# Performance work log

Measured on AMD Instinct MI355X. Metric: run time of the kernel, lower is better.

Reference implementation:

```python
import jax, jax.numpy as jnp
import numpy as np

B, Q, K = 16, 100, 100
H, DM = 8, 512
DK = DM // H          # 64, per-head dim (= Attention embed_dim)
MID = 32              # mid_dim
EPS = 1e-5            # GroupNorm eps
NEG = -1000000000.0   # masked_fill value


def setup_inputs() -> dict:
    key = jax.random.key(0)
    ks = jax.random.split(key, 32)
    def n(k, shape, s=0.02):
        return jax.random.normal(k, shape, jnp.float32) * s
    inp = {
        "query": jax.random.normal(ks[0], (B, Q, DM), jnp.float32),
        "key":   jax.random.normal(ks[1], (B, K, DM), jnp.float32),
        "value": jax.random.normal(ks[2], (B, K, DM), jnp.float32),
        "mask":  jnp.ones((B, Q, K), jnp.float32),
        # 4 input projections: Linear(DM,DM) -> CELU -> GroupNorm(H, DM)
        "Wq1": n(ks[3], (DM, DM)), "bq1": jnp.zeros((DM,), jnp.float32),
        "gw1": jnp.ones((DM,), jnp.float32), "gb1": jnp.zeros((DM,), jnp.float32),
        "Wk":  n(ks[4], (DM, DM)), "bk":  jnp.zeros((DM,), jnp.float32),
        "gwk": jnp.ones((DM,), jnp.float32), "gbk": jnp.zeros((DM,), jnp.float32),
        "Wq2": n(ks[5], (DM, DM)), "bq2": jnp.zeros((DM,), jnp.float32),
        "gw2": jnp.ones((DM,), jnp.float32), "gb2": jnp.zeros((DM,), jnp.float32),
        "Wv":  n(ks[6], (DM, DM)), "bv":  jnp.zeros((DM,), jnp.float32),
        "gwv": jnp.ones((DM,), jnp.float32), "gbv": jnp.zeros((DM,), jnp.float32),
        # Attention MLPs (per-head, embed_dim = DK)
        "We":  n(ks[7], (MID, DK)), "be":  jnp.zeros((MID,), jnp.float32),
        "Ws":  n(ks[8], (1, MID)),  "bs":  jnp.zeros((1,), jnp.float32),
        "Wsq": n(ks[9], (DK, MID)), "bsq": jnp.zeros((DK,), jnp.float32),
    }
    return inp


def _proj(x, W, b, gw, gb):
    """Linear -> CELU -> GroupNorm(H groups over DM channels), then split heads.
    x: (B, L, DM) -> (B, H, L, DK)"""
    Bn, L, _ = x.shape
    y = jax.nn.celu(x.reshape(Bn * L, DM) @ W.T + b)
    yg = y.reshape(Bn * L, H, DK)
    mu = yg.mean(-1, keepdims=True)
    var = yg.var(-1, keepdims=True)
    yn = ((yg - mu) * jax.lax.rsqrt(var + EPS)).reshape(Bn * L, DM)
    yn = yn * gw + gb
    return yn.reshape(Bn, L, H, DK).transpose(0, 2, 1, 3)


def reference(query, key, value, mask,
              Wq1, bq1, gw1, gb1, Wk, bk, gwk, gbk,
              Wq2, bq2, gw2, gb2, Wv, bv, gwv, gbv,
              We, be, Ws, bs, Wsq, bsq):
    q1 = _proj(query, Wq1, bq1, gw1, gb1)   # (B,H,Q,DK)
    k  = _proj(key,   Wk,  bk,  gwk, gbk)   # (B,H,K,DK)
    q2 = _proj(query, Wq2, bq2, gw2, gb2)   # (B,H,Q,DK)
    v  = _proj(value, Wv,  bv,  gwv, gbv)   # (B,H,K,DK)

    m = mask[:, None]                        # (B,1,Q,K)
    # bilinear query-key map, embedded by Linear->ReLU (dropout=identity, eval)
    key_map = jnp.einsum('bhqd,bhkd->bhqkd', q1, k)          # (B,H,Q,K,DK)
    km = jax.nn.relu(jnp.einsum('bhqkd,md->bhqkm', key_map, We) + be)  # (B,H,Q,K,MID)

    alpha = jnp.einsum('bhqkm,m->bhqk', km, Ws[0]) + bs[0]   # (B,H,Q,K)
    alpha = jnp.where(m == 0, NEG, alpha)
    alpha = jax.nn.softmax(alpha, axis=-1)

    # masked mean pooling over K, then channel squeeze-excite
    pool = jnp.sum(km * m[..., None], axis=-2) / jnp.sum(m[..., None], axis=-2)  # (B,H,Q,MID)
    ch = jax.nn.sigmoid(pool @ Wsq.T + bsq)                  # (B,H,Q,DK)

    # spatial attention over val_map: sum_k alpha * (q2_d * v_kd) = q2 * (alpha @ v)
    sp = q2 * jnp.einsum('bhqk,bhkd->bhqd', alpha, v)        # (B,H,Q,DK)
    x = sp * ch
    return x.transpose(0, 2, 1, 3).reshape(x.shape[0], -1, DM)  # (B,Q,DM)
```

## Files before the change

### kernel.cpp

```cpp
#include <hip/hip_runtime.h>
#include <hip/hip_bf16.h>
#include <math.h>

#define H 8
#define DM 512
#define DK 64
#define MID 32
#define LL 100
#define EPS 1e-5f
#define NEGV -1000000000.0f

typedef unsigned short u16;
typedef __attribute__((ext_vector_type(8))) short short8b;
typedef __attribute__((ext_vector_type(16))) float f32x16;

#define MFMA32 __builtin_amdgcn_mfma_f32_32x32x16_bf16

__device__ __forceinline__ unsigned pkbf2(float a, float b) {
    union { __hip_bfloat162 h; unsigned u; } cv;
    cv.h = __float22bfloat162_rn(make_float2(a, b));
    return cv.u;
}
__device__ __forceinline__ u16 bfbits(float a) {
    union { __hip_bfloat16 b; u16 u; } cv;
    cv.b = __float2bfloat16(a);
    return cv.u;
}
__device__ __forceinline__ float bf2f(u16 u) {
    union { u16 u; __hip_bfloat16 b; } cv; cv.u = u;
    return __bfloat162float(cv.b);
}

__global__ __launch_bounds__(256) void cvt_kernel(
    const float* __restrict__ q, const float* __restrict__ k, const float* __restrict__ v,
    const float* __restrict__ w1, const float* __restrict__ wk,
    const float* __restrict__ w2, const float* __restrict__ wv,
    u16* __restrict__ qh, u16* __restrict__ qlo, u16* __restrict__ kh, u16* __restrict__ klo,
    u16* __restrict__ vh, u16* __restrict__ vlo,
    u16* __restrict__ w1h, u16* __restrict__ w1l, u16* __restrict__ wkh, u16* __restrict__ wkl,
    u16* __restrict__ w2h, u16* __restrict__ w2l, u16* __restrict__ wvh, u16* __restrict__ wvl)
{
    int g = blockIdx.x * 256 + threadIdx.x;
    const float* src; u16 *dh, *dl; int off;
    if (g < 307200) {
        int a = g / 102400;
        off = g - a * 102400;
        src = a == 0 ? q : (a == 1 ? k : v);
        dh  = a == 0 ? qh : (a == 1 ? kh : vh);
        dl  = a == 0 ? qlo : (a == 1 ? klo : vlo);
    } else {
        int gg = g - 307200;
        int a = gg >> 15;
        off = gg & 32767;
        src = a == 0 ? w1 : (a == 1 ? wk : (a == 2 ? w2 : wv));
        dh  = a == 0 ? w1h : (a == 1 ? wkh : (a == 2 ? w2h : wvh));
        dl  = a == 0 ? w1l : (a == 1 ? wkl : (a == 2 ? w2l : wvl));
    }
    const int rr = off & 31, hf = (off >> 5) & 1, kb = (off >> 6) & 31, tile = off >> 11;
    const float* sp = src + ((size_t)(tile * 32 + rr)) * 512 + kb * 16 + hf * 8;
    float4 x0 = *(const float4*)sp;
    float4 x1 = *(const float4*)(sp + 4);
    float xs[8] = {x0.x, x0.y, x0.z, x0.w, x1.x, x1.y, x1.z, x1.w};
    u16 hb[8], lb[8];
    #pragma unroll
    for (int j = 0; j < 8; ++j) {
        hb[j] = bfbits(xs[j]);
        lb[j] = bfbits(xs[j] - bf2f(hb[j]));
    }
    ushort4 h0; h0.x = hb[0]; h0.y = hb[1]; h0.z = hb[2]; h0.w = hb[3];
    ushort4 h1; h1.x = hb[4]; h1.y = hb[5]; h1.z = hb[6]; h1.w = hb[7];
    ushort4 l0; l0.x = lb[0]; l0.y = lb[1]; l0.z = lb[2]; l0.w = lb[3];
    ushort4 l1; l1.x = lb[4]; l1.y = lb[5]; l1.z = lb[6]; l1.w = lb[7];
    *(ushort4*)(dh + (size_t)off * 8)     = h0;
    *(ushort4*)(dh + (size_t)off * 8 + 4) = h1;
    *(ushort4*)(dl + (size_t)off * 8)     = l0;
    *(ushort4*)(dl + (size_t)off * 8 + 4) = l1;
}

__global__ __launch_bounds__(256) void proj_kernel(
    const u16* __restrict__ qh, const u16* __restrict__ qlo,
    const u16* __restrict__ kh, const u16* __restrict__ klo,
    const u16* __restrict__ vh, const u16* __restrict__ vlo,
    const u16* __restrict__ w1h, const u16* __restrict__ w1l,
    const u16* __restrict__ wkh, const u16* __restrict__ wkl,
    const u16* __restrict__ w2h, const u16* __restrict__ w2l,
    const u16* __restrict__ wvh, const u16* __restrict__ wvl,
    const float* __restrict__ bq1, const float* __restrict__ gw1, const float* __restrict__ gb1,
    const float* __restrict__ bk , const float* __restrict__ gwk, const float* __restrict__ gbk,
    const float* __restrict__ bq2, const float* __restrict__ gw2, const float* __restrict__ gb2,
    const float* __restrict__ bv , const float* __restrict__ gwv, const float* __restrict__ gbv,
    float* __restrict__ q1o, u16* __restrict__ kbf,
    float* __restrict__ q2o, u16* __restrict__ vtbf)
{
    __shared__ float lds_s[4][32];
    __shared__ float lds_q[4][32];

    const int rt = blockIdx.x;
    const int ct = blockIdx.y;
    const int p  = blockIdx.z;
    const int t = threadIdx.x, w = t >> 6, lane = t & 63, ql = lane & 31, hf = lane >> 5;
    const int wr = w >> 1, wc = w & 1;

    const u16 *Xhg, *Xlg, *Whg, *Wlg; const float *bias, *gw, *gb;
    if (p == 0)      { Xhg=qh; Xlg=qlo; Whg=w1h; Wlg=w1l; bias=bq1; gw=gw1; gb=gb1; }
    else if (p == 1) { Xhg=kh; Xlg=klo; Whg=wkh; Wlg=wkl; bias=bk;  gw=gwk; gb=gbk; }
    else if (p == 2) { Xhg=qh; Xlg=qlo; Whg=w2h; Wlg=w2l; bias=bq2; gw=gw2; gb=gb2; }
    else             { Xhg=vh; Xlg=vlo; Whg=wvh; Wlg=wvl; bias=bv;  gw=gwv; gb=gbv; }

    const int rtile = rt * 2 + wr;
    const int ctile = ct * 2 + wc;
    const u16* pAh = Xhg + (size_t)rtile * 16384 + hf * 256 + ql * 8;
    const u16* pAl = Xlg + (size_t)rtile * 16384 + hf * 256 + ql * 8;
    const u16* pBh = Whg + (size_t)ctile * 16384 + hf * 256 + ql * 8;
    const u16* pBl = Wlg + (size_t)ctile * 16384 + hf * 256 + ql * 8;

    f32x16 acc = {0.f,0.f,0.f,0.f,0.f,0.f,0.f,0.f,0.f,0.f,0.f,0.f,0.f,0.f,0.f,0.f};
    #pragma unroll 4
    for (int kb = 0; kb < 32; ++kb) {
        short8b Ah = *(const short8b*)(pAh + kb * 512);
        short8b Al = *(const short8b*)(pAl + kb * 512);
        short8b Bh = *(const short8b*)(pBh + kb * 512);
        short8b Bl = *(const short8b*)(pBl + kb * 512);
        acc = MFMA32(Ah, Bh, acc, 0, 0, 0);
        acc = MFMA32(Ah, Bl, acc, 0, 0, 0);
        acc = MFMA32(Al, Bh, acc, 0, 0, 0);
    }

    const int colg = ct * 64 + wc * 32 + ql;
    const float bv_ = bias[colg];
    const float gwc = gw[colg], gbc = gb[colg];
    float y[16], s[16], sq[16];
    #pragma unroll
    for (int r = 0; r < 16; ++r) {
        float x = acc[r] + bv_;
        x = x > 0.f ? x : expm1f(x);
        y[r] = x; s[r] = x; sq[r] = x * x;
    }
    #pragma unroll
    for (int off = 1; off < 32; off <<= 1) {
        #pragma unroll
        for (int r = 0; r < 16; ++r) {
            s[r]  += __shfl_xor(s[r],  off, 64);
            sq[r] += __shfl_xor(sq[r], off, 64);
        }
    }
    if (ql == 0) {
        #pragma unroll
        for (int r = 0; r < 16; ++r) {
            int row = (r & 3) + 8 * (r >> 2) + 4 * hf;
            lds_s[w][row] = s[r]; lds_q[w][row] = sq[r];
        }
    }
    __syncthreads();
    const int wp = w ^ 1;
    const int hh = ct, dk = wc * 32 + ql;
    const int r0 = rt * 64 + wr * 32;
    #pragma unroll
    for (int r = 0; r < 16; ++r) {
        int row = (r & 3) + 8 * (r >> 2) + 4 * hf;
        float sum = lds_s[w][row] + lds_s[wp][row];
        float ssq = lds_q[w][row] + lds_q[wp][row];
        float mu  = sum * (1.f / 64.f);
        float var = ssq * (1.f / 64.f) - mu * mu;
        float inv = rsqrtf(var + EPS);
        float yn  = (y[r] - mu) * inv * gwc + gbc;
        int rg = r0 + row;
        int b = rg / 100;
        int l = rg - b * 100;
        size_t bh = (size_t)(b * H + hh);
        if (p == 0)      q1o[(bh * 100 + l) * 64 + dk] = yn;
        else if (p == 2) q2o[(bh * 100 + l) * 64 + dk] = yn;
        else if (p == 1) kbf[(bh * 128 + l) * 64 + dk] = bfbits(yn);
        else             vtbf[(bh * 64 + dk) * 128 + l] = bfbits(yn);
    }
}

__global__ __launch_bounds__(256, 2) void attn_kernel(
    const float* __restrict__ q1o, const u16* __restrict__ kbf,
    const float* __restrict__ q2o, const u16* __restrict__ vtbf,
    const float* __restrict__ mask,
    const float* __restrict__ We, const float* __restrict__ be,
    const float* __restrict__ Wsv, const float* __restrict__ bs,
    const float* __restrict__ Wsq, const float* __restrict__ bsq,
    float* __restrict__ out)
{
    __shared__ float lds_We[32 * 64];
    __shared__ float lds_score[128 * 33];
    __shared__ float lds_pool[2][32 * 33];
    __shared__ float lds_of[2][16 * 64];
    __shared__ float lds_mx[2][32], lds_se[2][32], lds_ms[2][32];

    const int bh = blockIdx.x, b = bh >> 3, h = bh & 7, qt = blockIdx.y;
    const int tid = threadIdx.x;
    const int w = tid >> 6, lane = tid & 63;
    const int wk = w >> 1, wm = w & 1;
    const int ql = lane & 31, hf = lane >> 5;
    const int q0 = qt * 32, q = q0 + ql;
    const int qc = q < 100 ? q : 99;

    for (int i = tid * 4; i < 2048; i += 1024)
        *(float4*)(lds_We + i) = *(const float4*)(We + i);
    for (int i = tid; i < 2 * 32 * 33; i += 256)
        ((float*)lds_pool)[i] = 0.f;

    const u16* kb = kbf + (size_t)bh * 128 * 64;
    short8b A[2][4];
    #pragma unroll
    for (int mtl = 0; mtl < 2; ++mtl)
        #pragma unroll
        for (int ks = 0; ks < 4; ++ks)
            A[mtl][ks] = *(const short8b*)(kb + (size_t)((2 * wk + mtl) * 32 + ql) * 64 + ks * 16 + hf * 8);

    float q1r[4][8];
    const float* q1p = q1o + ((size_t)bh * 100 + qc) * 64;
    #pragma unroll
    for (int ks = 0; ks < 4; ++ks) {
        float4 u0 = *(const float4*)(q1p + ks * 16 + hf * 8);
        float4 u1 = *(const float4*)(q1p + ks * 16 + hf * 8 + 4);
        q1r[ks][0] = u0.x; q1r[ks][1] = u0.y; q1r[ks][2] = u0.z; q1r[ks][3] = u0.w;
        q1r[ks][4] = u1.x; q1r[ks][5] = u1.y; q1r[ks][6] = u1.z; q1r[ks][7] = u1.w;
    }
    const float bsv = bs[0];

    float sc[2][16];
    #pragma unroll
    for (int mtl = 0; mtl < 2; ++mtl)
        #pragma unroll
        for (int r = 0; r < 16; ++r) sc[mtl][r] = 0.f;

    __syncthreads();

    for (int mi = 0; mi < 16; ++mi) {
        const int m = wm * 16 + mi;
        const float bem = be[m], wsm = Wsv[m];
        short8b Bf[4];
        #pragma unroll
        for (int ks = 0; ks < 4; ++ks) {
            const float* wp_ = lds_We + m * 64 + ks * 16 + hf * 8;
            float4 w0 = *(const float4*)(wp_);
            float4 w1 = *(const float4*)(wp_ + 4);
            union { unsigned u[4]; short8b v; } pk;
            pk.u[0] = pkbf2(w0.x * q1r[ks][0], w0.y * q1r[ks][1]);
            pk.u[1] = pkbf2(w0.z * q1r[ks][2], w0.w * q1r[ks][3]);
            pk.u[2] = pkbf2(w1.x * q1r[ks][4], w1.y * q1r[ks][5]);
            pk.u[3] = pkbf2(w1.z * q1r[ks][6], w1.w * q1r[ks][7]);
            Bf[ks] = pk.v;
        }
        #pragma unroll
        for (int mtl = 0; mtl < 2; ++mtl) {
            const int mt = 2 * wk + mtl;
            f32x16 c = {0.f,0.f,0.f,0.f,0.f,0.f,0.f,0.f,0.f,0.f,0.f,0.f,0.f,0.f,0.f,0.f};
            c = MFMA32(A[mtl][0], Bf[0], c, 0, 0, 0);
            c = MFMA32(A[mtl][1], Bf[1], c, 0, 0, 0);
            c = MFMA32(A[mtl][2], Bf[2], c, 0, 0, 0);
            c = MFMA32(A[mtl][3], Bf[3], c, 0, 0, 0);
            float psum = 0.f, psum4 = 0.f;
            #pragma unroll
            for (int r = 0; r < 16; ++r) {
                float tv = fmaxf(c[r] + bem, 0.f);
                sc[mtl][r] = fmaf(tv, wsm, sc[mtl][r]);
                if (mt != 3) psum += tv;
                else if (r < 4) psum4 += tv;
            }
            if (mt == 3) psum = (hf == 0) ? psum4 : 0.f;
            psum += __shfl_xor(psum, 32, 64);
            if (hf == 0) lds_pool[wk][ql * 33 + m] += psum;
        }
    }

    float msum = 0.f;
    const float* mrow = mask + ((size_t)b * 100 + qc) * 100;
    #pragma unroll
    for (int mtl = 0; mtl < 2; ++mtl) {
        const int mt = 2 * wk + mtl;
        #pragma unroll
        for (int g = 0; g < 4; ++g) {
            int k0 = mt * 32 + g * 8 + hf * 4;
            if (k0 < 100) {
                float4 mk = *(const float4*)(mrow + k0);
                msum += mk.x + mk.y + mk.z + mk.w;
                if (mk.x == 0.f) sc[mtl][g * 4 + 0] = NEGV;
                if (mk.y == 0.f) sc[mtl][g * 4 + 1] = NEGV;
                if (mk.z == 0.f) sc[mtl][g * 4 + 2] = NEGV;
                if (mk.w == 0.f) sc[mtl][g * 4 + 3] = NEGV;
            } else {
                sc[mtl][g * 4 + 0] = -INFINITY; sc[mtl][g * 4 + 1] = -INFINITY;
                sc[mtl][g * 4 + 2] = -INFINITY; sc[mtl][g * 4 + 3] = -INFINITY;
            }
        }
    }
    msum += __shfl_xor(msum, 32, 64);

    if (wm == 0) {
        #pragma unroll
        for (int mtl = 0; mtl < 2; ++mtl)
            #pragma unroll
            for (int r = 0; r < 16; ++r) {
                int row = (2 * wk + mtl) * 32 + (r & 3) + 8 * (r >> 2) + 4 * hf;
                lds_score[row * 33 + ql] = sc[mtl][r];
            }
    }
    __syncthreads();
    if (wm == 1) {
        #pragma unroll
        for (int mtl = 0; mtl < 2; ++mtl)
            #pragma unroll
            for (int r = 0; r < 16; ++r) {
                int row = (2 * wk + mtl) * 32 + (r & 3) + 8 * (r >> 2) + 4 * hf;
                lds_score[row * 33 + ql] += sc[mtl][r];
            }
    }
    __syncthreads();

    float mx = -INFINITY;
    #pragma unroll
    for (int mtl = 0; mtl < 2; ++mtl)
        #pragma unroll
        for (int r = 0; r < 16; ++r) {
            int row = (2 * wk + mtl) * 32 + (r & 3) + 8 * (r >> 2) + 4 * hf;
            float sv = lds_score[row * 33 + ql] + bsv;
            sc[mtl][r] = sv;
            mx = fmaxf(mx, sv);
        }
    mx = fmaxf(mx, __shfl_xor(mx, 32, 64));
    if (hf == 0 && wm == 0) { lds_mx[wk][ql] = mx; lds_ms[wk][ql] = msum; }
    __syncthreads();
    mx = fmaxf(lds_mx[0][ql], lds_mx[1][ql]);
    const float msumT = lds_ms[0][ql] + lds_ms[1][ql];
    float se = 0.f;
    #pragma unroll
    for (int mtl = 0; mtl < 2; ++mtl)
        #pragma unroll
        for (int r = 0; r < 16; ++r) {
            float ev = expf(sc[mtl][r] - mx);
            sc[mtl][r] = ev;
            se += ev;
        }
    se += __shfl_xor(se, 32, 64);
    if (hf == 0 && wm == 0) lds_se[wk][ql] = se;
    __syncthreads();
    const float inv_se = 1.f / (lds_se[0][ql] + lds_se[1][ql]);
    #pragma unroll
    for (int mtl = 0; mtl < 2; ++mtl)
        #pragma unroll
        for (int r = 0; r < 16; ++r) sc[mtl][r] *= inv_se;

    const int nks = 4 - wk;
    short8b A2[4];
    #pragma unroll
    for (int ksl = 0; ksl < 4; ++ksl) {
        if (ksl < nks) {
            const int s_ = ksl & 1, mtl = ksl >> 1;
            unsigned a0 = pkbf2(sc[mtl][8 * s_ + 0], sc[mtl][8 * s_ + 1]);
            unsigned a1 = pkbf2(sc[mtl][8 * s_ + 2], sc[mtl][8 * s_ + 3]);
            unsigned b0 = pkbf2(sc[mtl][8 * s_ + 4], sc[mtl][8 * s_ + 5]);
            unsigned b1 = pkbf2(sc[mtl][8 * s_ + 6], sc[mtl][8 * s_ + 7]);
            unsigned o0 = hf ? b0 : a0, o1 = hf ? b1 : a1;
            unsigned s0 = hf ? a0 : b0, s1 = hf ? a1 : b1;
            unsigned r0_ = (unsigned)__shfl_xor((int)s0, 32, 64);
            unsigned r1_ = (unsigned)__shfl_xor((int)s1, 32, 64);
            union { unsigned u[4]; short8b v; } pk;
            pk.u[0] = hf ? r0_ : o0;  pk.u[1] = hf ? r1_ : o1;
            pk.u[2] = hf ? o0 : r0_;  pk.u[3] = hf ? o1 : r1_;
            A2[ksl] = pk.v;
        }
    }

    const u16* vb = vtbf + (size_t)bh * 64 * 128 + (size_t)(wm * 32 + ql) * 128;
    f32x16 o = {0.f,0.f,0.f,0.f,0.f,0.f,0.f,0.f,0.f,0.f,0.f,0.f,0.f,0.f,0.f,0.f};
    #pragma unroll
    for (int ksl = 0; ksl < 4; ++ksl) {
        if (ksl < nks) {
            short8b vf = *(const short8b*)(vb + (4 * wk + ksl) * 16 + hf * 8);
            o = MFMA32(A2[ksl], vf, o, 0, 0, 0);
        }
    }

    if (wk == 0) {
        #pragma unroll
        for (int r = 0; r < 16; ++r) lds_of[wm][r * 64 + lane] = o[r];
    }
    __syncthreads();
    if (wk == 1) {
        #pragma unroll
        for (int r = 0; r < 16; ++r) o[r] += lds_of[wm][r * 64 + lane];

        const float invm = 1.f / msumT;
        short8b A3[2], B3[2];
        #pragma unroll
        for (int ks = 0; ks < 2; ++ks) {
            const float* p0_ = lds_pool[0] + ql * 33 + ks * 16 + hf * 8;
            const float* p1_ = lds_pool[1] + ql * 33 + ks * 16 + hf * 8;
            union { unsigned u[4]; short8b v; } pk;
            pk.u[0] = pkbf2((p0_[0]+p1_[0])*invm, (p0_[1]+p1_[1])*invm);
            pk.u[1] = pkbf2((p0_[2]+p1_[2])*invm, (p0_[3]+p1_[3])*invm);
            pk.u[2] = pkbf2((p0_[4]+p1_[4])*invm, (p0_[5]+p1_[5])*invm);
            pk.u[3] = pkbf2((p0_[6]+p1_[6])*invm, (p0_[7]+p1_[7])*invm);
            A3[ks] = pk.v;
            const float* wqp = Wsq + (size_t)(wm * 32 + ql) * 32 + ks * 16 + hf * 8;
            float4 c0 = *(const float4*)(wqp);
            float4 c1 = *(const float4*)(wqp + 4);
            union { unsigned u[4]; short8b v; } pk2;
            pk2.u[0] = pkbf2(c0.x, c0.y); pk2.u[1] = pkbf2(c0.z, c0.w);
            pk2.u[2] = pkbf2(c1.x, c1.y); pk2.u[3] = pkbf2(c1.z, c1.w);
            B3[ks] = pk2.v;
        }
        f32x16 z = {0.f,0.f,0.f,0.f,0.f,0.f,0.f,0.f,0.f,0.f,0.f,0.f,0.f,0.f,0.f,0.f};
        z = MFMA32(A3[0], B3[0], z, 0, 0, 0);
        z = MFMA32(A3[1], B3[1], z, 0, 0, 0);

        const float bsqv = bsq[wm * 32 + ql];
        const float* q2p = q2o + (size_t)bh * 100 * 64;
        const int dcol = wm * 32 + ql;
        #pragma unroll
        for (int r = 0; r < 16; ++r) {
            int qr = q0 + (r & 3) + 8 * (r >> 2) + 4 * hf;
            if (qr < 100) {
                float chv = 1.f / (1.f + expf(-(z[r] + bsqv)));
                float ov  = o[r] * chv * q2p[(size_t)qr * 64 + dcol];
                out[((size_t)(b * 100 + qr)) * DM + h * 64 + dcol] = ov;
            }
        }
    }
}

extern "C" void kernel_launch(void* const* d_in, const int* in_sizes, int n_in,
                              void* d_out, int out_size, void* d_ws, size_t ws_size,
                              hipStream_t stream)
{
    const float* query = (const float*)d_in[0];
    const float* key   = (const float*)d_in[1];
    const float* value = (const float*)d_in[2];
    const float* mask  = (const float*)d_in[3];
    const float* Wq1 = (const float*)d_in[4];
    const float* bq1 = (const float*)d_in[5];
    const float* gw1 = (const float*)d_in[6];
    const float* gb1 = (const float*)d_in[7];
    const float* Wk  = (const float*)d_in[8];
    const float* bk  = (const float*)d_in[9];
    const float* gwk = (const float*)d_in[10];
    const float* gbk = (const float*)d_in[11];
    const float* Wq2 = (const float*)d_in[12];
    const float* bq2 = (const float*)d_in[13];
    const float* gw2 = (const float*)d_in[14];
    const float* gb2 = (const float*)d_in[15];
    const float* Wv  = (const float*)d_in[16];
    const float* bv  = (const float*)d_in[17];
    const float* gwv = (const float*)d_in[18];
    const float* gbv = (const float*)d_in[19];
    const float* We  = (const float*)d_in[20];
    const float* be  = (const float*)d_in[21];
    const float* Ws  = (const float*)d_in[22];
    const float* bs  = (const float*)d_in[23];
    const float* Wsq = (const float*)d_in[24];
    const float* bsq = (const float*)d_in[25];

    float* wsf = (float*)d_ws;
    float* q1o = wsf;
    float* q2o = wsf + 819200;
    u16* kbf   = (u16*)(wsf + 1638400);
    u16* vtbf  = kbf + 1048576;
    u16* c0    = vtbf + 1048576;
    u16 *qh = c0, *qlo = qh + 819200, *khh = qlo + 819200, *klo = khh + 819200,
        *vhh = klo + 819200, *vlo = vhh + 819200;
    u16* wbase = vlo + 819200;
    u16 *w1h = wbase,          *w1l = w1h + 262144,
        *wkh = w1l + 262144,   *wkl = wkh + 262144,
        *w2h = wkl + 262144,   *w2l = w2h + 262144,
        *wvh = w2l + 262144,   *wvl = wvh + 262144;

    cvt_kernel<<<1712, 256, 0, stream>>>(query, key, value, Wq1, Wk, Wq2, Wv,
        qh, qlo, khh, klo, vhh, vlo, w1h, w1l, wkh, wkl, w2h, w2l, wvh, wvl);

    dim3 g1(25, 8, 4);
    proj_kernel<<<g1, 256, 0, stream>>>(
        qh, qlo, khh, klo, vhh, vlo, w1h, w1l, wkh, wkl, w2h, w2l, wvh, wvl,
        bq1, gw1, gb1, bk, gwk, gbk, bq2, gw2, gb2, bv, gwv, gbv,
        q1o, kbf, q2o, vtbf);

    dim3 g2(128, 4);
    attn_kernel<<<g2, 256, 0, stream>>>(q1o, kbf, q2o, vtbf, mask,
        We, be, Ws, bs, Wsq, bsq, (float*)d_out);
}
```

Baseline: 182.2 us.

## Restructure projection GEMM: one wave per head, register prefetch, XCD-aware block mapping

The projection kernel now gives each wave a full 32x64 head slice using two accumulators that share the A fragment. This lets the GroupNorm reduction stay inside the wave, so the LDS exchange and __syncthreads go away. Global fragment loads are software-prefetched one k-step ahead, and the 1D grid is mapped so each XCD sees a contiguous set of projection/column pairs. The convert kernel uses a 2D grid to drop the per-thread division and select logic. The cost is more registers per wave and fewer threads per block.

New measurement: 178.3 us. -2.1%, faster.

```diff
diff --git a/kernel.cpp b/kernel.cpp
--- a/kernel.cpp
+++ b/kernel.cpp
@@ -40,22 +40,19 @@
     u16* __restrict__ w1h, u16* __restrict__ w1l, u16* __restrict__ wkh, u16* __restrict__ wkl,
     u16* __restrict__ w2h, u16* __restrict__ w2l, u16* __restrict__ wvh, u16* __restrict__ wvl)
 {
-    int g = blockIdx.x * 256 + threadIdx.x;
-    const float* src; u16 *dh, *dl; int off;
-    if (g < 307200) {
-        int a = g / 102400;
-        off = g - a * 102400;
-        src = a == 0 ? q : (a == 1 ? k : v);
-        dh  = a == 0 ? qh : (a == 1 ? kh : vh);
-        dl  = a == 0 ? qlo : (a == 1 ? klo : vlo);
-    } else {
-        int gg = g - 307200;
-        int a = gg >> 15;
-        off = gg & 32767;
-        src = a == 0 ? w1 : (a == 1 ? wk : (a == 2 ? w2 : wv));
-        dh  = a == 0 ? w1h : (a == 1 ? wkh : (a == 2 ? w2h : wvh));
-        dl  = a == 0 ? w1l : (a == 1 ? wkl : (a == 2 ? w2l : wvl));
-    }
+    const int a = blockIdx.y;
+    if (a >= 3 && blockIdx.x >= 128) return;
+    const float* src; u16 *dh, *dl;
+    switch (a) {
+        case 0: src = q;  dh = qh;  dl = qlo; break;
+        case 1: src = k;  dh = kh;  dl = klo; break;
+        case 2: src = v;  dh = vh;  dl = vlo; break;
+        case 3: src = w1; dh = w1h; dl = w1l; break;
+        case 4: src = wk; dh = wkh; dl = wkl; break;
+        case 5: src = w2; dh = w2h; dl = w2l; break;
+        default: src = wv; dh = wvh; dl = wvl; break;
+    }
+    const int off = blockIdx.x * 256 + threadIdx.x;
     const int rr = off & 31, hf = (off >> 5) & 1, kb = (off >> 6) & 31, tile = off >> 11;
     const float* sp = src + ((size_t)(tile * 32 + rr)) * 512 + kb * 16 + hf * 8;
     float4 x0 = *(const float4*)sp;
@@ -77,7 +74,8 @@
     *(ushort4*)(dl + (size_t)off * 8 + 4) = l1;
 }
 
-__global__ __launch_bounds__(256) void proj_kernel(
+#define LDF(p_, kb_) (*(const short8b*)((p_) + (kb_) * 512))
+__global__ __launch_bounds__(128) void proj_kernel(
     const u16* __restrict__ qh, const u16* __restrict__ qlo,
     const u16* __restrict__ kh, const u16* __restrict__ klo,
     const u16* __restrict__ vh, const u16* __restrict__ vlo,
@@ -92,14 +90,13 @@
     float* __restrict__ q1o, u16* __restrict__ kbf,
     float* __restrict__ q2o, u16* __restrict__ vtbf)
 {
-    __shared__ float lds_s[4][32];
-    __shared__ float lds_q[4][32];
-
-    const int rt = blockIdx.x;
-    const int ct = blockIdx.y;
-    const int p  = blockIdx.z;
-    const int t = threadIdx.x, w = t >> 6, lane = t & 63, ql = lane & 31, hf = lane >> 5;
-    const int wr = w >> 1, wc = w & 1;
+    const int bid = blockIdx.x;
+    const int x = bid & 7, j = bid >> 3;
+    const int rt = j % 50;
+    const int pair = x * 2 + j / 50;
+    const int p = pair >> 2, ct = pair & 3;
+
+    const int t = threadIdx.x, wc = t >> 6, lane = t & 63, ql = lane & 31, hf = lane >> 5;
 
     const u16 *Xhg, *Xlg, *Whg, *Wlg; const float *bias, *gw, *gb;
     if (p == 0)      { Xhg=qh; Xlg=qlo; Whg=w1h; Wlg=w1l; bias=bq1; gw=gw1; gb=gb1; }
@@ -107,34 +104,54 @@
     else if (p == 2) { Xhg=qh; Xlg=qlo; Whg=w2h; Wlg=w2l; bias=bq2; gw=gw2; gb=gb2; }
     else             { Xhg=vh; Xlg=vlo; Whg=wvh; Wlg=wvl; bias=bv;  gw=gwv; gb=gbv; }
 
-    const int rtile = rt * 2 + wr;
-    const int ctile = ct * 2 + wc;
-    const u16* pAh = Xhg + (size_t)rtile * 16384 + hf * 256 + ql * 8;
-    const u16* pAl = Xlg + (size_t)rtile * 16384 + hf * 256 + ql * 8;
-    const u16* pBh = Whg + (size_t)ctile * 16384 + hf * 256 + ql * 8;
-    const u16* pBl = Wlg + (size_t)ctile * 16384 + hf * 256 + ql * 8;
-
-    f32x16 acc = {0.f,0.f,0.f,0.f,0.f,0.f,0.f,0.f,0.f,0.f,0.f,0.f,0.f,0.f,0.f,0.f};
-    #pragma unroll 4
-    for (int kb = 0; kb < 32; ++kb) {
-        short8b Ah = *(const short8b*)(pAh + kb * 512);
-        short8b Al = *(const short8b*)(pAl + kb * 512);
-        short8b Bh = *(const short8b*)(pBh + kb * 512);
-        short8b Bl = *(const short8b*)(pBl + kb * 512);
-        acc = MFMA32(Ah, Bh, acc, 0, 0, 0);
-        acc = MFMA32(Ah, Bl, acc, 0, 0, 0);
-        acc = MFMA32(Al, Bh, acc, 0, 0, 0);
-    }
-
-    const int colg = ct * 64 + wc * 32 + ql;
-    const float bv_ = bias[colg];
-    const float gwc = gw[colg], gbc = gb[colg];
-    float y[16], s[16], sq[16];
+    const int ctile = ct * 4 + wc * 2;
+    const u16* pAh  = Xhg + (size_t)rt * 16384 + hf * 256 + ql * 8;
+    const u16* pAl  = Xlg + (size_t)rt * 16384 + hf * 256 + ql * 8;
+    const u16* pB0h = Whg + (size_t)ctile * 16384 + hf * 256 + ql * 8;
+    const u16* pB0l = Wlg + (size_t)ctile * 16384 + hf * 256 + ql * 8;
+    const u16* pB1h = pB0h + 16384;
+    const u16* pB1l = pB0l + 16384;
+
+    f32x16 acc0 = {0.f,0.f,0.f,0.f,0.f,0.f,0.f,0.f,0.f,0.f,0.f,0.f,0.f,0.f,0.f,0.f};
+    f32x16 acc1 = {0.f,0.f,0.f,0.f,0.f,0.f,0.f,0.f,0.f,0.f,0.f,0.f,0.f,0.f,0.f,0.f};
+
+    short8b cAh = LDF(pAh, 0), cAl = LDF(pAl, 0);
+    short8b cB0h = LDF(pB0h, 0), cB0l = LDF(pB0l, 0);
+    short8b cB1h = LDF(pB1h, 0), cB1l = LDF(pB1l, 0);
+
+    #pragma unroll 2
+    for (int kb = 0; kb < 31; ++kb) {
+        short8b nAh  = LDF(pAh,  kb + 1), nAl  = LDF(pAl,  kb + 1);
+        short8b nB0h = LDF(pB0h, kb + 1), nB0l = LDF(pB0l, kb + 1);
+        short8b nB1h = LDF(pB1h, kb + 1), nB1l = LDF(pB1l, kb + 1);
+        acc0 = MFMA32(cAh, cB0h, acc0, 0, 0, 0);
+        acc1 = MFMA32(cAh, cB1h, acc1, 0, 0, 0);
+        acc0 = MFMA32(cAh, cB0l, acc0, 0, 0, 0);
+        acc1 = MFMA32(cAh, cB1l, acc1, 0, 0, 0);
+        acc0 = MFMA32(cAl, cB0h, acc0, 0, 0, 0);
+        acc1 = MFMA32(cAl, cB1h, acc1, 0, 0, 0);
+        cAh = nAh; cAl = nAl; cB0h = nB0h; cB0l = nB0l; cB1h = nB1h; cB1l = nB1l;
+    }
+    acc0 = MFMA32(cAh, cB0h, acc0, 0, 0, 0);
+    acc1 = MFMA32(cAh, cB1h, acc1, 0, 0, 0);
+    acc0 = MFMA32(cAh, cB0l, acc0, 0, 0, 0);
+    acc1 = MFMA32(cAh, cB1l, acc1, 0, 0, 0);
+    acc0 = MFMA32(cAl, cB0h, acc0, 0, 0, 0);
+    acc1 = MFMA32(cAl, cB1h, acc1, 0, 0, 0);
+
+    const int c0 = ct * 128 + wc * 64 + ql;
+    const int c1 = c0 + 32;
+    const float b0 = bias[c0], b1 = bias[c1];
+    const float gw0 = gw[c0], gb0 = gb[c0], gw1_ = gw[c1], gb1_ = gb[c1];
+    float y0[16], y1[16], s[16], sq[16];
     #pragma unroll
     for (int r = 0; r < 16; ++r) {
-        float x = acc[r] + bv_;
-        x = x > 0.f ? x : expm1f(x);
-        y[r] = x; s[r] = x; sq[r] = x * x;
+        float a0 = acc0[r] + b0;
+        float a1 = acc1[r] + b1;
+        a0 = a0 > 0.f ? a0 : expm1f(a0);
+        a1 = a1 > 0.f ? a1 : expm1f(a1);
+        y0[r] = a0; y1[r] = a1;
+        s[r] = a0 + a1; sq[r] = a0 * a0 + a1 * a1;
     }
     #pragma unroll
     for (int off = 1; off < 32; off <<= 1) {
@@ -144,34 +161,32 @@
             sq[r] += __shfl_xor(sq[r], off, 64);
         }
     }
-    if (ql == 0) {
-        #pragma unroll
-        for (int r = 0; r < 16; ++r) {
-            int row = (r & 3) + 8 * (r >> 2) + 4 * hf;
-            lds_s[w][row] = s[r]; lds_q[w][row] = sq[r];
-        }
-    }
-    __syncthreads();
-    const int wp = w ^ 1;
-    const int hh = ct, dk = wc * 32 + ql;
-    const int r0 = rt * 64 + wr * 32;
+    const int hh = ct * 2 + wc;
     #pragma unroll
     for (int r = 0; r < 16; ++r) {
-        int row = (r & 3) + 8 * (r >> 2) + 4 * hf;
-        float sum = lds_s[w][row] + lds_s[wp][row];
-        float ssq = lds_q[w][row] + lds_q[wp][row];
-        float mu  = sum * (1.f / 64.f);
-        float var = ssq * (1.f / 64.f) - mu * mu;
-        float inv = rsqrtf(var + EPS);
-        float yn  = (y[r] - mu) * inv * gwc + gbc;
-        int rg = r0 + row;
-        int b = rg / 100;
-        int l = rg - b * 100;
-        size_t bh = (size_t)(b * H + hh);
-        if (p == 0)      q1o[(bh * 100 + l) * 64 + dk] = yn;
-        else if (p == 2) q2o[(bh * 100 + l) * 64 + dk] = yn;
-        else if (p == 1) kbf[(bh * 128 + l) * 64 + dk] = bfbits(yn);
-        else             vtbf[(bh * 64 + dk) * 128 + l] = bfbits(yn);
+        const float mu  = s[r] * (1.f / 64.f);
+        const float var = sq[r] * (1.f / 64.f) - mu * mu;
+        const float inv = rsqrtf(var + EPS);
+        const float yn0 = (y0[r] - mu) * inv * gw0 + gb0;
+        const float yn1 = (y1[r] - mu) * inv * gw1_ + gb1_;
+        const int row = (r & 3) + 8 * (r >> 2) + 4 * hf;
+        const int rg = rt * 32 + row;
+        const int b = rg / 100;
+        const int l = rg - b * 100;
+        const size_t bh = (size_t)(b * H + hh);
+        if (p == 0) {
+            q1o[(bh * 100 + l) * 64 + ql]      = yn0;
+            q1o[(bh * 100 + l) * 64 + 32 + ql] = yn1;
+        } else if (p == 2) {
+            q2o[(bh * 100 + l) * 64 + ql]      = yn0;
+            q2o[(bh * 100 + l) * 64 + 32 + ql] = yn1;
+        } else if (p == 1) {
+            kbf[(bh * 128 + l) * 64 + ql]      = bfbits(yn0);
+            kbf[(bh * 128 + l) * 64 + 32 + ql] = bfbits(yn1);
+        } else {
+            vtbf[(bh * 64 + ql) * 128 + l]      = bfbits(yn0);
+            vtbf[(bh * 64 + 32 + ql) * 128 + l] = bfbits(yn1);
+        }
     }
 }
 
@@ -469,11 +484,11 @@
         *w2h = wkl + 262144,   *w2l = w2h + 262144,
         *wvh = w2l + 262144,   *wvl = wvh + 262144;
 
-    cvt_kernel<<<1712, 256, 0, stream>>>(query, key, value, Wq1, Wk, Wq2, Wv,
+    dim3 gc(400, 7);
+    cvt_kernel<<<gc, 256, 0, stream>>>(query, key, value, Wq1, Wk, Wq2, Wv,
         qh, qlo, khh, klo, vhh, vlo, w1h, w1l, wkh, wkl, w2h, w2l, wvh, wvl);
 
-    dim3 g1(25, 8, 4);
-    proj_kernel<<<g1, 256, 0, stream>>>(
+    proj_kernel<<<800, 128, 0, stream>>>(
         qh, qlo, khh, klo, vhh, vlo, w1h, w1l, wkh, wkl, w2h, w2l, wvh, wvl,
         bq1, gw1, gb1, bk, gwk, gbk, bq2, gw2, gb2, bv, gwv, gbv,
         q1o, kbf, q2o, vtbf);
```
